# Performance work log

Hardware: AMD Instinct MI355X
Metric: run time of the kernel (lower is better)

## Reference

```python
import jax, jax.numpy as jnp
import numpy as np

NEG = -1e30

def setup_inputs() -> dict:
    key = jax.random.key(0)
    k = jax.random.split(key, 6)
    B, Lc, Lq, D = 16, 2048, 256, 256
    c = jax.random.normal(k[0], (B, Lc, D), dtype=jnp.float32)
    q = jax.random.normal(k[1], (B, Lq, D), dtype=jnp.float32)
    c_mask = jnp.ones((B, Lc), dtype=jnp.float32)
    q_mask = jnp.ones((B, Lq), dtype=jnp.float32)
    # xavier-uniform-ish scale for the similarity weights
    lim = float(np.sqrt(6.0 / (D + 1)))
    cq_weight = jax.random.uniform(k[2], (1, 1, D), jnp.float32, -lim, lim)
    c_weight = jax.random.uniform(k[3], (1, D), jnp.float32, -lim, lim)
    q_weight = jax.random.uniform(k[4], (1, D), jnp.float32, -lim, lim)
    bias = jnp.zeros((1,), dtype=jnp.float32)
    return {"c": c, "q": q, "c_mask": c_mask, "q_mask": q_mask,
            "cq_weight": cq_weight, "c_weight": c_weight,
            "q_weight": q_weight, "bias": bias}

def _masked_softmax(logits, mask):
    # mask: 1=keep, 0=pad; broadcast over logits' leading dims
    x = logits * mask + (1.0 - mask) * NEG
    return jax.nn.softmax(x, axis=-1)

def reference(c, q, c_mask, q_mask, cq_weight, c_weight, q_weight, bias):
    # trilinear similarity S[b,i,j] = w_c.c_i + w_q.q_j + (c_i*w_cq).q_j + b
    s0 = jnp.einsum('bid,od->bio', c, c_weight)              # [B,Lc,1]
    s1 = jnp.einsum('bjd,od->boj', q, q_weight)              # [B,1,Lq]
    s2 = jnp.einsum('bid,bjd->bij', c * cq_weight, q)        # [B,Lc,Lq]
    S = s0 + s1 + s2 + bias                                  # [B,Lc,Lq]
    S1 = _masked_softmax(S, q_mask[:, None, :])              # softmax over q
    C2Q = jnp.einsum('bij,bjd->bid', S1, q)                  # [B,Lc,D]
    S2t = _masked_softmax(jnp.swapaxes(S, 1, 2), c_mask[:, None, :])  # [B,Lq,Lc]
    S2 = jnp.einsum('bij,bjk->bik', S1, S2t)                 # [B,Lc,Lc]
    Q2C = jnp.einsum('bik,bkd->bid', S2, c)                  # [B,Lc,D]
    return jnp.concatenate((c, C2Q, c * C2Q, c * Q2C), axis=-1)
```

## Files before the change

### kernel.cpp

```cpp
#include <hip/hip_runtime.h>
#include <hip/hip_bf16.h>

#define NB 16
#define LC 2048
#define LQ 256
#define DD 256
#define NEGINF -1e30f

typedef __attribute__((ext_vector_type(8))) short bf16x8;
typedef __attribute__((ext_vector_type(4))) float f32x4;

#define MFMA16(a, b, c) __builtin_amdgcn_mfma_f32_16x16x32_bf16((a), (b), (c), 0, 0, 0)

typedef const unsigned int __attribute__((address_space(1))) glb_u32;
typedef unsigned int __attribute__((address_space(3))) lds_u32;

__device__ __forceinline__ void gload_lds16(const void* g, void* l) {
    __builtin_amdgcn_global_load_lds((glb_u32*)g, (lds_u32*)l, 16, 0, 0);
}

__device__ __forceinline__ short f2b(float x) {
    unsigned u = __float_as_uint(x);
    unsigned r = (u + 0x7fffu + ((u >> 16) & 1u)) >> 16;
    return (short)r;
}
__device__ __forceinline__ float b2f(short s) {
    return __uint_as_float(((unsigned)(unsigned short)s) << 16);
}

#define NCB (NB * LC / 8)
__global__ __launch_bounds__(256) void prep(
        const float* __restrict__ c, const float* __restrict__ q,
        const float* __restrict__ c_w, const float* __restrict__ cqw,
        const float* __restrict__ q_w, const float* __restrict__ bias,
        short* __restrict__ c16, float* __restrict__ s0c,
        short* __restrict__ qw16, short* __restrict__ qT16,
        float* __restrict__ s1q) {
    __shared__ float T[64][65];
    int t = threadIdx.x;
    if (blockIdx.x < NCB) {
        int row = blockIdx.x * 8 + (t >> 5);
        int k = t & 31;
        const float* src = c + (size_t)row * DD + k * 8;
        float4 v0 = *(const float4*)(src);
        float4 v1 = *(const float4*)(src + 4);
        float4 w0 = *(const float4*)(c_w + k * 8);
        float4 w1 = *(const float4*)(c_w + k * 8 + 4);
        float s = v0.x * w0.x + v0.y * w0.y + v0.z * w0.z + v0.w * w0.w
                + v1.x * w1.x + v1.y * w1.y + v1.z * w1.z + v1.w * w1.w;
        #pragma unroll
        for (int o = 16; o > 0; o >>= 1) s += __shfl_xor(s, o, 64);
        if (k == 0) s0c[row] = s;
        ushort4 o0, o1;
        o0.x = (unsigned short)f2b(v0.x); o0.y = (unsigned short)f2b(v0.y);
        o0.z = (unsigned short)f2b(v0.z); o0.w = (unsigned short)f2b(v0.w);
        o1.x = (unsigned short)f2b(v1.x); o1.y = (unsigned short)f2b(v1.y);
        o1.z = (unsigned short)f2b(v1.z); o1.w = (unsigned short)f2b(v1.w);
        ushort4* dst = (ushort4*)(c16 + (size_t)row * DD + k * 8);
        dst[0] = o0;
        dst[1] = o1;
    } else {
        int idx = blockIdx.x - NCB;
        int b = idx >> 2, j0 = (idx & 3) * 64;
        int dd = t & 63, rg = t >> 6;
        float acc[16];
        #pragma unroll
        for (int i = 0; i < 16; ++i) acc[i] = 0.f;
        for (int dc = 0; dc < 4; ++dc) {
            float wv = cqw[dc * 64 + dd];
            float qwv = q_w[dc * 64 + dd];
            #pragma unroll
            for (int rr = 0; rr < 16; ++rr) {
                int r = rg + 4 * rr;
                float v = q[((size_t)b * LQ + j0 + r) * DD + dc * 64 + dd];
                qw16[((size_t)b * LQ + j0 + r) * DD + dc * 64 + dd] = f2b(v * wv);
                acc[rr] += v * qwv;
                T[dd][r] = v;
            }
            __syncthreads();
            int jj = t & 63;
            for (int dw = t >> 6; dw < 64; dw += 4)
                qT16[((size_t)b * DD + dc * 64 + dw) * LQ + j0 + jj] = f2b(T[dw][jj]);
            __syncthreads();
        }
        float bv = bias[0];
        #pragma unroll
        for (int rr = 0; rr < 16; ++rr) {
            float s = acc[rr];
            #pragma unroll
            for (int o = 32; o > 0; o >>= 1) s += __shfl_xor(s, o, 64);
            if (dd == 0) s1q[b * LQ + j0 + rg + 4 * rr] = s + bv;
        }
    }
}

__global__ __launch_bounds__(512) void k1_S(
        const short* __restrict__ c16, const short* __restrict__ qw16,
        const float* __restrict__ cmask, const float* __restrict__ qmask,
        const float* __restrict__ s0c, const float* __restrict__ s1q,
        short* __restrict__ P1b, float* __restrict__ rowC,
        float* __restrict__ pm, float* __restrict__ ps) {
    __shared__ short As[128 * 64];
    __shared__ short Bs[256 * 64];
    __shared__ float rmLds[128 * 4];
    __shared__ float rsLds[128 * 4];
    __shared__ float rowCLds[128];
    int b  = blockIdx.y;
    int i0 = blockIdx.x * 128;
    int t = threadIdx.x;
    int l = t & 63, w = t >> 6;
    int wr = w >> 2, wc = w & 3;

    f32x4 acc[4][4];
    #pragma unroll
    for (int m = 0; m < 4; ++m)
        #pragma unroll
        for (int n = 0; n < 4; ++n) acc[m][n] = (f32x4){0.f, 0.f, 0.f, 0.f};

    const short* Ag = c16  + ((size_t)b * LC + i0) * DD;
    const short* Bg = qw16 + ((size_t)b * LQ) * DD;
    int lrow = l >> 3;
    int lcolsw = ((l & 7) ^ lrow) * 8;

    for (int kt = 0; kt < DD; kt += 64) {
        __syncthreads();
        #pragma unroll
        for (int r = 0; r < 2; ++r) {
            int chunk = r * 8 + w;
            int row = chunk * 8 + lrow;
            gload_lds16(Ag + (size_t)row * DD + kt + lcolsw, As + chunk * 512);
        }
        #pragma unroll
        for (int r = 0; r < 4; ++r) {
            int chunk = r * 8 + w;
            int row = chunk * 8 + lrow;
            gload_lds16(Bg + (size_t)row * DD + kt + lcolsw, Bs + chunk * 512);
        }
        __syncthreads();
        #pragma unroll
        for (int kf = 0; kf < 2; ++kf) {
            bf16x8 a[4], bb[4];
            #pragma unroll
            for (int m = 0; m < 4; ++m) {
                int row = wr * 64 + m * 16 + (l & 15);
                int byte = row * 128 + kf * 64 + (l >> 4) * 16;
                a[m] = *(const bf16x8*)((const char*)As + (byte ^ ((row & 7) << 4)));
            }
            #pragma unroll
            for (int n = 0; n < 4; ++n) {
                int row = wc * 64 + n * 16 + (l & 15);
                int byte = row * 128 + kf * 64 + (l >> 4) * 16;
                bb[n] = *(const bf16x8*)((const char*)Bs + (byte ^ ((row & 7) << 4)));
            }
            #pragma unroll
            for (int m = 0; m < 4; ++m)
                #pragma unroll
                for (int n = 0; n < 4; ++n)
                    acc[m][n] = MFMA16(a[m], bb[n], acc[m][n]);
        }
    }

    float s1v[4], qmv[4], negq[4];
    #pragma unroll
    for (int n = 0; n < 4; ++n) {
        int j = wc * 64 + n * 16 + (l & 15);
        s1v[n] = s1q[b * LQ + j];
        qmv[n] = qmask[b * LQ + j];
        negq[n] = (1.f - qmv[n]) * NEGINF;
    }
    float s0r[4][4], cmr[4][4];
    #pragma unroll
    for (int m = 0; m < 4; ++m)
        #pragma unroll
        for (int reg = 0; reg < 4; ++reg) {
            int il = wr * 64 + m * 16 + (l >> 4) * 4 + reg;
            s0r[m][reg] = s0c[b * LC + i0 + il];
            cmr[m][reg] = cmask[b * LC + i0 + il];
        }
    #pragma unroll
    for (int m = 0; m < 4; ++m)
        #pragma unroll
        for (int n = 0; n < 4; ++n)
            #pragma unroll
            for (int reg = 0; reg < 4; ++reg) {
                float v = acc[m][n][reg] + s0r[m][reg] + s1v[n];
                acc[m][n][reg] = b2f(f2b(v));
            }

    #pragma unroll
    for (int n = 0; n < 4; ++n) {
        float x2v[16];
        float mx = NEGINF;
        #pragma unroll
        for (int m = 0; m < 4; ++m)
            #pragma unroll
            for (int reg = 0; reg < 4; ++reg) {
                float cm = cmr[m][reg];
                float x2 = acc[m][n][reg] * cm + (1.f - cm) * NEGINF;
                x2v[m * 4 + reg] = x2;
                mx = fmaxf(mx, x2);
            }
        float ss = 0.f;
        #pragma unroll
        for (int e = 0; e < 16; ++e) ss += __expf(x2v[e] - mx);
        #pragma unroll
        for (int off = 16; off <= 32; off <<= 1) {
            float om = __shfl_xor(mx, off, 64);
            float os = __shfl_xor(ss, off, 64);
            float nm = fmaxf(mx, om);
            ss = ss * __expf(mx - nm) + os * __expf(om - nm);
            mx = nm;
        }
        if (l < 16) {
            size_t idx = ((size_t)b * 32 + blockIdx.x * 2 + wr) * LQ + wc * 64 + n * 16 + l;
            pm[idx] = mx;
            ps[idx] = ss;
        }
    }

    #pragma unroll
    for (int m = 0; m < 4; ++m)
        #pragma unroll
        for (int reg = 0; reg < 4; ++reg) {
            float mx = NEGINF;
            #pragma unroll
            for (int n = 0; n < 4; ++n)
                mx = fmaxf(mx, fmaf(acc[m][n][reg], qmv[n], negq[n]));
            #pragma unroll
            for (int o = 1; o <= 8; o <<= 1) mx = fmaxf(mx, __shfl_xor(mx, o, 64));
            float ss = 0.f;
            #pragma unroll
            for (int n = 0; n < 4; ++n)
                ss += __expf(fmaf(acc[m][n][reg], qmv[n], negq[n]) - mx);
            #pragma unroll
            for (int o = 1; o <= 8; o <<= 1) ss += __shfl_xor(ss, o, 64);
            if ((l & 15) == 0) {
                int row = wr * 64 + m * 16 + (l >> 4) * 4 + reg;
                rmLds[row * 4 + wc] = mx;
                rsLds[row * 4 + wc] = ss;
            }
        }
    __syncthreads();
    if (t < 128) {
        float m0 = rmLds[t * 4 + 0], m1 = rmLds[t * 4 + 1];
        float m2 = rmLds[t * 4 + 2], m3 = rmLds[t * 4 + 3];
        float mm = fmaxf(fmaxf(m0, m1), fmaxf(m2, m3));
        float ss = rsLds[t * 4 + 0] * __expf(m0 - mm)
                 + rsLds[t * 4 + 1] * __expf(m1 - mm)
                 + rsLds[t * 4 + 2] * __expf(m2 - mm)
                 + rsLds[t * 4 + 3] * __expf(m3 - mm);
        float rc = mm + logf(ss);
        rowCLds[t] = rc;
        rowC[(size_t)b * LC + i0 + t] = rc;
    }
    __syncthreads();

    float rCv[4][4];
    #pragma unroll
    for (int m = 0; m < 4; ++m)
        #pragma unroll
        for (int reg = 0; reg < 4; ++reg)
            rCv[m][reg] = rowCLds[wr * 64 + m * 16 + (l >> 4) * 4 + reg];
    #pragma unroll
    for (int m = 0; m < 4; ++m)
        #pragma unroll
        for (int n = 0; n < 4; ++n)
            #pragma unroll
            for (int reg = 0; reg < 4; ++reg) {
                float p = __expf(fmaf(acc[m][n][reg], qmv[n], negq[n]) - rCv[m][reg]);
                int il = wr * 64 + m * 16 + (l >> 4) * 4 + reg;
                int j = wc * 64 + n * 16 + (l & 15);
                P1b[((size_t)b * LC + i0 + il) * LQ + j] = f2b(p);
            }
}

#define K3S 72
__global__ __launch_bounds__(256) void k3_A2C(
        const short* __restrict__ c16, const short* __restrict__ P1b,
        const float* __restrict__ cmask, const float* __restrict__ rowC,
        float* __restrict__ p3) {
    __shared__ short As[128 * K3S];
    __shared__ short Bs[128 * K3S];
    int b  = blockIdx.z;
    int ks = blockIdx.y;
    int d0 = (blockIdx.x >> 1) * 128;
    int j0 = (blockIdx.x & 1) * 128;
    int t = threadIdx.x, l = t & 63, w = t >> 6;
    int wr = w >> 1, wc = w & 1;

    f32x4 acc[4][4];
    #pragma unroll
    for (int m = 0; m < 4; ++m)
        #pragma unroll
        for (int n = 0; n < 4; ++n) acc[m][n] = (f32x4){0.f, 0.f, 0.f, 0.f};

    int ii = t >> 2;
    int c4 = (t & 3) * 8;

    for (int k0 = ks * 512; k0 < ks * 512 + 512; k0 += 64) {
        __syncthreads();
        float wgt = cmask[b * LC + k0 + ii] * __expf(rowC[(size_t)b * LC + k0 + ii]);
        #pragma unroll
        for (int e = 0; e < 4; ++e) {
            int dpos = c4 + e * 32;
            bf16x8 av = *(const bf16x8*)(c16 +
                    ((size_t)(b * LC + k0 + ii)) * DD + d0 + dpos);
            #pragma unroll
            for (int g = 0; g < 8; ++g) As[(dpos + g) * K3S + ii] = av[g];

            int jpos = c4 + e * 32;
            bf16x8 p8 = *(const bf16x8*)(P1b +
                    ((size_t)(b * LC + k0 + ii)) * LQ + j0 + jpos);
            #pragma unroll
            for (int g = 0; g < 8; ++g)
                Bs[(jpos + g) * K3S + ii] = f2b(b2f(p8[g]) * wgt);
        }
        __syncthreads();
        #pragma unroll
        for (int kf = 0; kf < 2; ++kf) {
            bf16x8 a[4], bb[4];
            #pragma unroll
            for (int m = 0; m < 4; ++m) {
                int row = wr * 64 + m * 16 + (l & 15);
                a[m] = *(const bf16x8*)((const char*)As +
                        row * (K3S * 2) + kf * 64 + (l >> 4) * 16);
            }
            #pragma unroll
            for (int n = 0; n < 4; ++n) {
                int row = wc * 64 + n * 16 + (l & 15);
                bb[n] = *(const bf16x8*)((const char*)Bs +
                        row * (K3S * 2) + kf * 64 + (l >> 4) * 16);
            }
            #pragma unroll
            for (int m = 0; m < 4; ++m)
                #pragma unroll
                for (int n = 0; n < 4; ++n)
                    acc[m][n] = MFMA16(a[m], bb[n], acc[m][n]);
        }
    }
    float* P = p3 + (((size_t)b * 4 + ks) * 4 + blockIdx.x) * 16384;
    #pragma unroll
    for (int m = 0; m < 4; ++m)
        #pragma unroll
        for (int n = 0; n < 4; ++n)
            #pragma unroll
            for (int reg = 0; reg < 4; ++reg) {
                int ld = wr * 64 + m * 16 + (l >> 4) * 4 + reg;
                int lj = wc * 64 + n * 16 + (l & 15);
                P[ld * 128 + lj] = acc[m][n][reg];
            }
}

__global__ __launch_bounds__(256) void k3r_reduce(
        const float* __restrict__ p3,
        const float* __restrict__ pm, const float* __restrict__ ps,
        short* __restrict__ A2CT) {
    __shared__ float colCs[256];
    int b = blockIdx.y;
    int t = threadIdx.x;
    {
        float m = NEGINF, s = 0.f;
        for (int ch = 0; ch < 32; ++ch) {
            float pmv = pm[((size_t)b * 32 + ch) * LQ + t];
            float psv = ps[((size_t)b * 32 + ch) * LQ + t];
            float mn = fmaxf(m, pmv);
            s = s * __expf(m - mn) + psv * __expf(pmv - mn);
            m = mn;
        }
        colCs[t] = m + logf(s);
    }
    __syncthreads();
    int linear = blockIdx.x * 256 + t;
    int d = linear >> 6;
    int j4 = (linear & 63) * 4;
    int tile = (d >> 7) * 2 + (j4 >> 7);
    int ld = d & 127, lj = j4 & 127;
    const float* base = p3 + (((size_t)b * 4) * 4 + tile) * 16384 + ld * 128 + lj;
    float4 s = {0.f, 0.f, 0.f, 0.f};
    #pragma unroll
    for (int ks = 0; ks < 4; ++ks) {
        float4 v = *(const float4*)(base + (size_t)ks * 4 * 16384);
        s.x += v.x; s.y += v.y; s.z += v.z; s.w += v.w;
    }
    s.x *= __expf(-colCs[j4 + 0]);
    s.y *= __expf(-colCs[j4 + 1]);
    s.z *= __expf(-colCs[j4 + 2]);
    s.w *= __expf(-colCs[j4 + 3]);
    short4 o;
    o.x = f2b(s.x); o.y = f2b(s.y); o.z = f2b(s.z); o.w = f2b(s.w);
    *(short4*)(A2CT + ((size_t)b * DD + d) * LQ + j4) = o;
}

__global__ __launch_bounds__(256) void k4_out(
        const short* __restrict__ P1b, const short* __restrict__ qT16,
        const short* __restrict__ A2CT, const float* __restrict__ c,
        float* __restrict__ out) {
    int b = blockIdx.y, i0 = blockIdx.x * 64;
    int t = threadIdx.x, l = t & 63, w = t >> 6;
    int d0w = w * 64;

    f32x4 acc1[4][4], acc2[4][4];
    #pragma unroll
    for (int m = 0; m < 4; ++m)
        #pragma unroll
        for (int n = 0; n < 4; ++n) {
            acc1[m][n] = (f32x4){0.f, 0.f, 0.f, 0.f};
            acc2[m][n] = (f32x4){0.f, 0.f, 0.f, 0.f};
        }
    const short* Sr  = P1b  + ((size_t)b * LC + i0) * LQ;
    const short* qTb = qT16 + (size_t)b * DD * LQ;
    const short* aTb = A2CT + (size_t)b * DD * LQ;

    #pragma unroll 2
    for (int kf = 0; kf < 8; ++kf) {
        int j8 = kf * 32 + (l >> 4) * 8;
        bf16x8 a[4];
        #pragma unroll
        for (int m = 0; m < 4; ++m)
            a[m] = *(const bf16x8*)(Sr + (size_t)(m * 16 + (l & 15)) * LQ + j8);
        #pragma unroll
        for (int n = 0; n < 4; ++n) {
            int d = d0w + n * 16 + (l & 15);
            size_t off = (size_t)d * LQ + j8;
            bf16x8 bq = *(const bf16x8*)(qTb + off);
            bf16x8 ba = *(const bf16x8*)(aTb + off);
            #pragma unroll
            for (int m = 0; m < 4; ++m) {
                acc1[m][n] = MFMA16(a[m], bq, acc1[m][n]);
                acc2[m][n] = MFMA16(a[m], ba, acc2[m][n]);
            }
        }
    }
    #pragma unroll
    for (int m = 0; m < 4; ++m)
        #pragma unroll
        for (int n = 0; n < 4; ++n)
            #pragma unroll
            for (int reg = 0; reg < 4; ++reg) {
                int i = i0 + m * 16 + (l >> 4) * 4 + reg;
                int d = d0w + n * 16 + (l & 15);
                float cv = c[((size_t)b * LC + i) * DD + d];
                size_t ob = ((size_t)b * LC + i) * (size_t)(4 * DD);
                float v1 = acc1[m][n][reg], v2 = acc2[m][n][reg];
                out[ob + d]           = cv;
                out[ob + 256 + d]     = v1;
                out[ob + 512 + d]     = cv * v1;
                out[ob + 768 + d]     = cv * v2;
            }
}

extern "C" void kernel_launch(void* const* d_in, const int* in_sizes, int n_in,
                              void* d_out, int out_size, void* d_ws, size_t ws_size,
                              hipStream_t stream) {
    const float* c     = (const float*)d_in[0];
    const float* q     = (const float*)d_in[1];
    const float* cmask = (const float*)d_in[2];
    const float* qmask = (const float*)d_in[3];
    const float* cqw   = (const float*)d_in[4];
    const float* c_w   = (const float*)d_in[5];
    const float* q_w   = (const float*)d_in[6];
    const float* bias  = (const float*)d_in[7];
    float* out = (float*)d_out;

    char* w = (char*)d_ws;
    short* P1b   = (short*)(w);
    short* c16   = (short*)(w + 16777216);
    short* qw16  = (short*)(w + 33554432);
    short* qT16  = (short*)(w + 35651584);
    short* A2CT  = (short*)(w + 37748736);
    float* s0c   = (float*)(w + 39845888);
    float* s1q   = (float*)(w + 39976960);
    float* pm    = (float*)(w + 39993344);
    float* ps    = (float*)(w + 40517632);
    float* rowC  = (float*)(w + 41041920);
    float* p3    = (float*)(w + 41172992);

    prep<<<dim3(NCB + NB * LQ / 64), dim3(256), 0, stream>>>(
        c, q, c_w, cqw, q_w, bias, c16, s0c, qw16, qT16, s1q);
    k1_S<<<dim3(LC / 128, NB), dim3(512), 0, stream>>>(
        c16, qw16, cmask, qmask, s0c, s1q, P1b, rowC, pm, ps);
    k3_A2C<<<dim3(4, 4, NB), dim3(256), 0, stream>>>(
        c16, P1b, cmask, rowC, p3);
    k3r_reduce<<<dim3(64, NB), dim3(256), 0, stream>>>(p3, pm, ps, A2CT);
    k4_out<<<dim3(LC / 64, NB), dim3(256), 0, stream>>>(
        P1b, qT16, A2CT, c, out);
}
```

Baseline: 118.8 us.

## Swizzle k3 LDS layout and stage k4 epilogue through LDS for vector stores

In the k3 kernel, the transposed LDS tiles As/Bs now use an XOR swizzle of the column index keyed by row group, on both the writes and the MFMA operand reads. This is meant to cut LDS bank conflicts. In k4_out, the accumulators are staged through shared memory one 16-row slice at a time, so each thread reads c and writes the four output segments as float4. This replaces scattered scalar global stores. It adds extra __syncthreads and LDS traffic.

```diff
diff --git a/kernel.cpp b/kernel.cpp
--- a/kernel.cpp
+++ b/kernel.cpp
@@ -303,33 +303,38 @@
         #pragma unroll
         for (int e = 0; e < 4; ++e) {
             int dpos = c4 + e * 32;
+            int iiA = ii ^ (((dpos >> 3) & 7) << 3);
             bf16x8 av = *(const bf16x8*)(c16 +
                     ((size_t)(b * LC + k0 + ii)) * DD + d0 + dpos);
             #pragma unroll
-            for (int g = 0; g < 8; ++g) As[(dpos + g) * K3S + ii] = av[g];
+            for (int g = 0; g < 8; ++g) As[(dpos + g) * K3S + iiA] = av[g];
 
             int jpos = c4 + e * 32;
+            int iiB = ii ^ (((jpos >> 3) & 7) << 3);
             bf16x8 p8 = *(const bf16x8*)(P1b +
                     ((size_t)(b * LC + k0 + ii)) * LQ + j0 + jpos);
             #pragma unroll
             for (int g = 0; g < 8; ++g)
-                Bs[(jpos + g) * K3S + ii] = f2b(b2f(p8[g]) * wgt);
+                Bs[(jpos + g) * K3S + iiB] = f2b(b2f(p8[g]) * wgt);
         }
         __syncthreads();
         #pragma unroll
         for (int kf = 0; kf < 2; ++kf) {
             bf16x8 a[4], bb[4];
+            int colL = kf * 32 + (l >> 4) * 8;
             #pragma unroll
             for (int m = 0; m < 4; ++m) {
                 int row = wr * 64 + m * 16 + (l & 15);
+                int colP = colL ^ (((row >> 3) & 7) << 3);
                 a[m] = *(const bf16x8*)((const char*)As +
-                        row * (K3S * 2) + kf * 64 + (l >> 4) * 16);
+                        row * (K3S * 2) + colP * 2);
             }
             #pragma unroll
             for (int n = 0; n < 4; ++n) {
                 int row = wc * 64 + n * 16 + (l & 15);
+                int colP = colL ^ (((row >> 3) & 7) << 3);
                 bb[n] = *(const bf16x8*)((const char*)Bs +
-                        row * (K3S * 2) + kf * 64 + (l >> 4) * 16);
+                        row * (K3S * 2) + colP * 2);
             }
             #pragma unroll
             for (int m = 0; m < 4; ++m)
@@ -395,6 +400,8 @@
         const short* __restrict__ P1b, const short* __restrict__ qT16,
         const short* __restrict__ A2CT, const float* __restrict__ c,
         float* __restrict__ out) {
+    __shared__ float Lo1[16][260];
+    __shared__ float Lo2[16][260];
     int b = blockIdx.y, i0 = blockIdx.x * 64;
     int t = threadIdx.x, l = t & 63, w = t >> 6;
     int d0w = w * 64;
@@ -431,22 +438,38 @@
             }
         }
     }
-    #pragma unroll
-    for (int m = 0; m < 4; ++m)
-        #pragma unroll
-        for (int n = 0; n < 4; ++n)
+
+    const float* cb = c + (size_t)b * LC * DD;
+    #pragma unroll
+    for (int m = 0; m < 4; ++m) {
+        __syncthreads();
+        #pragma unroll
+        for (int n = 0; n < 4; ++n) {
+            int col = d0w + n * 16 + (l & 15);
             #pragma unroll
             for (int reg = 0; reg < 4; ++reg) {
-                int i = i0 + m * 16 + (l >> 4) * 4 + reg;
-                int d = d0w + n * 16 + (l & 15);
-                float cv = c[((size_t)b * LC + i) * DD + d];
-                size_t ob = ((size_t)b * LC + i) * (size_t)(4 * DD);
-                float v1 = acc1[m][n][reg], v2 = acc2[m][n][reg];
-                out[ob + d]           = cv;
-                out[ob + 256 + d]     = v1;
-                out[ob + 512 + d]     = cv * v1;
-                out[ob + 768 + d]     = cv * v2;
-            }
+                int row = (l >> 4) * 4 + reg;
+                Lo1[row][col] = acc1[m][n][reg];
+                Lo2[row][col] = acc2[m][n][reg];
+            }
+        }
+        __syncthreads();
+        #pragma unroll
+        for (int rr = 0; rr < 4; ++rr) {
+            int row = w * 4 + rr;
+            int i = i0 + m * 16 + row;
+            float4 f1 = *(const float4*)&Lo1[row][l * 4];
+            float4 f2 = *(const float4*)&Lo2[row][l * 4];
+            float4 cv = *(const float4*)(cb + (size_t)i * DD + l * 4);
+            size_t ob = ((size_t)b * LC + i) * (size_t)(4 * DD);
+            float4 p1 = {cv.x * f1.x, cv.y * f1.y, cv.z * f1.z, cv.w * f1.w};
+            float4 p2 = {cv.x * f2.x, cv.y * f2.y, cv.z * f2.z, cv.w * f2.w};
+            *(float4*)(out + ob + l * 4)       = cv;
+            *(float4*)(out + ob + 256 + l * 4) = f1;
+            *(float4*)(out + ob + 512 + l * 4) = p1;
+            *(float4*)(out + ob + 768 + l * 4) = p2;
+        }
+    }
 }
 
 extern "C" void kernel_launch(void* const* d_in, const int* in_sizes, int n_in,
```

Result: no change. 120.8 us (+1.7%).
